# Kernel optimization log

Measured on AMD Instinct MI355X. Metric: run time of the kernel, lower is better.

## Reference

```python
import jax, jax.numpy as jnp
import numpy as np

NEG = -1e9  # max-semiring 'zero' / structural mask value


def _cky_max(pot, lengths):
    """Max-plus CKY inside pass (torch_struct CKY_CRF with MaxSemiring).

    pot: [B, N, N] label-maxed span potentials, pot[b, i, j] = score of span (i, j).
    Returns [B] best binary-tree score for each sequence of given length.
    betaA[b, i, w]      = best score of span starting at i with width w (span [i, i+w]).
    betaB[b, j, N-1-w]  = best score of span ending at j with width w.
    """
    B, N, _ = pot.shape
    term = jnp.diagonal(pot, axis1=1, axis2=2)  # [B, N] width-0 spans
    betaA = jnp.full((B, N, N), NEG, dtype=pot.dtype).at[:, :, 0].set(term)
    betaB = jnp.full((B, N, N), NEG, dtype=pot.dtype).at[:, :, N - 1].set(term)
    for w in range(1, N):
        Y = betaA[:, : N - w, :w]       # [B, N-w, w] left children, widths 0..w-1
        Z = betaB[:, w:, N - w:]        # [B, N-w, w] right children (matching splits)
        span = jnp.diagonal(pot, offset=w, axis1=1, axis2=2)  # [B, N-w] pot[b, i, i+w]
        new = jnp.max(Y + Z, axis=-1) + span
        betaA = betaA.at[:, : N - w, w].set(new)
        betaB = betaB.at[:, w:, N - w - 1].set(new)
    final = betaA[:, 0, :]  # [B, N]: final[b, l-1] = best tree over [0, l-1]
    return final[jnp.arange(B), lengths - 1]


def setup_inputs() -> dict:
    key = jax.random.key(0)
    k1, k2 = jax.random.split(key)
    B, N, L = 64, 128, 32
    logits = jax.random.normal(k1, (B, N, N, L), dtype=jnp.float32)
    labels = jax.random.randint(k2, (B, N, N), 0, L, dtype=jnp.int64)
    return {"logits": logits, "labels": labels}


def reference(logits, labels):
    B, N, _, L = logits.shape
    gold_event = jax.nn.one_hot(jnp.maximum(labels, 0), L, dtype=logits.dtype)
    logits = logits - logits[..., :1]
    lengths = jnp.sum(labels[:, 0, :] != -100, axis=-1)
    augment = 1.0 - gold_event
    # force_root_constituent=True: forbid non-constituent root span
    augment = augment.at[jnp.arange(B), 0, lengths - 1, 0].add(-1e9)
    pot = jnp.max(logits + augment, axis=-1)  # max-semiring sum over label dim
    pred_score = _cky_max(pot, lengths)                      # [B]
    gold_score = jnp.sum(logits * gold_event, axis=(1, 2, 3))  # [B]
    margin_losses = jax.nn.relu(pred_score - gold_score)
    return jnp.mean(margin_losses)
```

## Files before the change

### kernel.cpp

```cpp
#include <hip/hip_runtime.h>

#define BATCH 64
#define SEQ   128
#define NLAB  32
#define NEGF  -3.0e38f
#define PA    132

__device__ __forceinline__ void bar_k(int K) {
    switch (K) {
    case 0: asm volatile("s_waitcnt lgkmcnt(0)" ::: "memory"); break;
    case 1: asm volatile("s_waitcnt lgkmcnt(1)" ::: "memory"); break;
    case 2: asm volatile("s_waitcnt lgkmcnt(2)" ::: "memory"); break;
    case 3: asm volatile("s_waitcnt lgkmcnt(3)" ::: "memory"); break;
    case 4: asm volatile("s_waitcnt lgkmcnt(4)" ::: "memory"); break;
    case 5: asm volatile("s_waitcnt lgkmcnt(5)" ::: "memory"); break;
    case 6: asm volatile("s_waitcnt lgkmcnt(6)" ::: "memory"); break;
    default: asm volatile("s_waitcnt lgkmcnt(7)" ::: "memory"); break;
    }
    __builtin_amdgcn_s_barrier();
}

__global__ __launch_bounds__(256) void pot_gold_kernel(
    const float* __restrict__ logits, const int* __restrict__ labels,
    float* __restrict__ pot, float* __restrict__ gpart, float* __restrict__ out)
{
    const int tid = threadIdx.x;
    const int wave = tid >> 6, lane = tid & 63;
    __shared__ __align__(16) float LP[4 * 16 * 36];
    __shared__ float gred[4];
    __shared__ int s_len;
    float* W = LP + wave * (16 * 36);

    const int block_cell0 = blockIdx.x * 256;
    const int b = block_cell0 >> 14;
    const bool has_row0 = (blockIdx.x & 63) == 0;

    if (blockIdx.x == 0 && tid == 0) out[0] = 0.0f;

    if (has_row0 && tid < 64) {
        const size_t base = (size_t)b << 14;
        int cnt = (labels[base + tid] != -100) + (labels[base + 64 + tid] != -100);
        #pragma unroll
        for (int d = 32; d; d >>= 1) cnt += __shfl_down(cnt, d, 64);
        if (tid == 0) s_len = cnt;
    }
    __syncthreads();
    const int len = has_row0 ? s_len : -1;

    float gacc = 0.0f;
    const int wave_cell0 = block_cell0 + wave * 64;

    #pragma unroll
    for (int chunk = 0; chunk < 4; ++chunk) {
        const int c0 = wave_cell0 + chunk * 16;
        const float4* src = reinterpret_cast<const float4*>(logits) + ((size_t)c0 << 3);
        const float4 f0 = src[lane];
        const float4 f1 = src[lane + 64];
        const int lv = (lane < 16) ? labels[c0 + lane] : 0;

        {
            const int cA = lane >> 3, tA = lane & 7;
            *reinterpret_cast<float4*>(W + cA * 36 + tA * 4) = f0;
            const int q1 = lane + 64;
            const int cB = q1 >> 3, tB = q1 & 7;
            *reinterpret_cast<float4*>(W + cB * 36 + tB * 4) = f1;
        }
        const int c = lane >> 2, u = lane & 3;
        const float4 r0 = *reinterpret_cast<const float4*>(W + c * 36 + u * 8);
        const float4 r1 = *reinterpret_cast<const float4*>(W + c * 36 + u * 8 + 4);

        int lab = __shfl(lv, c, 64);
        if (lab < 0) lab = 0;
        const float l0 = __shfl(r0.x, c << 2, 64);

        const int cell = c0 + c;
        const int ci = (cell >> 7) & (SEQ - 1);
        const int cj = cell & (SEQ - 1);
        const bool special = (ci == 0) && (cj == len - 1);

        const float vv[8] = { r0.x, r0.y, r0.z, r0.w, r1.x, r1.y, r1.z, r1.w };
        float m = NEGF, g = 0.0f;
        #pragma unroll
        for (int e = 0; e < 8; ++e) {
            const int l = u * 8 + e;
            const float r = vv[e] - l0;
            const bool isg = (l == lab);
            g = isg ? r : g;
            float cand = r + (isg ? 0.0f : 1.0f);
            if (l == 0 && special) cand -= 1.0e9f;
            m = fmaxf(m, cand);
        }
        m = fmaxf(m, __shfl_xor(m, 1, 64));
        m = fmaxf(m, __shfl_xor(m, 2, 64));
        g += __shfl_xor(g, 1, 64);
        g += __shfl_xor(g, 2, 64);
        if (u == 0) {
            pot[cell] = m;
            gacc += g;
        }
    }

    #pragma unroll
    for (int d = 1; d < 64; d <<= 1) gacc += __shfl_xor(gacc, d, 64);
    if (lane == 0) gred[wave] = gacc;
    __syncthreads();
    if (tid == 0)
        gpart[blockIdx.x] = gred[0] + gred[1] + gred[2] + gred[3];
}

__global__ __launch_bounds__(512, 1) void cky_kernel(
    const float* __restrict__ pot, const float* __restrict__ gpart,
    const int* __restrict__ labels, float* __restrict__ out)
{
    const int b = blockIdx.x;
    const int tid = threadIdx.x;
    const float* p = pot + (size_t)b * SEQ * SEQ;

    __shared__ __align__(16) float A[SEQ * PA];
    __shared__ __align__(16) float Bt[SEQ * PA];
    __shared__ int s_len;
    __shared__ float s_gold;

    if (tid < 64) {
        const size_t base = (size_t)b << 14;
        int cnt = (labels[base + tid] != -100) + (labels[base + 64 + tid] != -100);
        #pragma unroll
        for (int d = 32; d; d >>= 1) cnt += __shfl_down(cnt, d, 64);
        if (tid == 0) s_len = cnt;
    } else if (tid < 128) {
        float g = gpart[b * 64 + (tid - 64)];
        #pragma unroll
        for (int d = 32; d; d >>= 1) g += __shfl_down(g, d, 64);
        if (tid == 64) s_gold = g;
    }

    {
        const float4* p4 = reinterpret_cast<const float4*>(p);
        float4 vb[8];
        #pragma unroll
        for (int t = 0; t < 8; ++t) vb[t] = p4[tid + 512 * t];
        #pragma unroll
        for (int t = 0; t < 8; ++t) {
            const int qi = tid + 512 * t;
            const int i0 = qi >> 5;
            const int j0 = (qi & 31) << 2;
            const float vv[4] = { vb[t].x, vb[t].y, vb[t].z, vb[t].w };
            #pragma unroll
            for (int c2 = 0; c2 < 4; ++c2) {
                const int j = j0 + c2;
                if (j >= i0) {
                    A[i0 * PA + (j - i0)] = vv[c2];
                    Bt[j * PA + (SEQ - 1 - (j - i0))] = vv[c2];
                }
            }
        }
    }
    __syncthreads();

    const int i = tid >> 2, s = tid & 3;
    float alo[16], av[16], pv[16], md[16];
    float bo_p[16], bf_p[12];

    #pragma unroll
    for (int t = 0; t < 4; ++t) {
        const float4 v = *reinterpret_cast<const float4*>(&A[i * PA + 4 * t]);
        pv[4*t] = v.x; pv[4*t+1] = v.y; pv[4*t+2] = v.z; pv[4*t+3] = v.w;
    }
    av[0] = pv[0];
    #pragma unroll
    for (int d = 1; d < 16; ++d) {
        const int j = i + d;
        const int tf = (d - 1) >> 2;
        const int jr = (j < SEQ) ? j : SEQ - 1;
        float bff[4];
        {
            const float4 u = *reinterpret_cast<const float4*>(&Bt[jr * PA + 124 - 4 * tf]);
            bff[0] = u.w; bff[1] = u.z; bff[2] = u.y; bff[3] = u.x;
        }
        float e[16];
        #pragma unroll
        for (int m = 0; m < d; ++m)
            e[m] = av[d - 1 - m] + ((m < 4 * tf) ? bo_p[m] : bff[m - 4 * tf]);
        #pragma unroll
        for (int stp = 1; stp < 16; stp <<= 1) {
            #pragma unroll
            for (int m = 0; m + stp < d; m += 2 * stp)
                e[m] = fmaxf(e[m], e[m + stp]);
        }
        const float val = e[0] + pv[d];
        av[d] = val;
        if (j < SEQ && s == 0) {
            A[i * PA + d] = val;
            Bt[j * PA + (SEQ - 1 - d)] = val;
        }
        __builtin_amdgcn_sched_barrier(0);
        if (d < 15) {
            int jp = j + 1; if (jp >= SEQ) jp = SEQ - 1;
            const int tfn = d >> 2;
            #pragma unroll
            for (int t = 0; t < 4; ++t) {
                if (t < tfn) {
                    const float4 v = *reinterpret_cast<const float4*>(&Bt[jp * PA + 124 - 4 * t]);
                    bo_p[4*t] = v.w; bo_p[4*t+1] = v.z; bo_p[4*t+2] = v.y; bo_p[4*t+3] = v.x;
                }
            }
            bar_k(tfn);
        } else {
            bar_k(0);
        }
    }
    #pragma unroll
    for (int k = 0; k < 16; ++k) alo[k] = av[k];

    for (int W = 16; W < SEQ; W += 16) {
        #pragma unroll
        for (int t = 0; t < 4; ++t) {
            const float4 v = *reinterpret_cast<const float4*>(&A[i * PA + W + 4 * t]);
            pv[4*t] = v.x; pv[4*t+1] = v.y; pv[4*t+2] = v.z; pv[4*t+3] = v.w;
        }
        #pragma unroll
        for (int d = 0; d < 16; ++d) md[d] = NEGF;

        {
            const int k0 = s << 2;
            const float4 a = *reinterpret_cast<const float4*>(&A[i * PA + k0]);
            const float aa[4] = { a.x, a.y, a.z, a.w };
            #pragma unroll
            for (int d = 0; d < 16; ++d) {
                const int j = i + W + d;
                if (j < SEQ) {
                    const float* bp = &Bt[j * PA + (SEQ - W - d) + k0];
                    float b0, b1, b2, b3;
                    if ((d & 3) == 0) {
                        const float4 v = *reinterpret_cast<const float4*>(bp);
                        b0 = v.x; b1 = v.y; b2 = v.z; b3 = v.w;
                    } else if ((d & 3) == 2) {
                        const float2 v0 = *reinterpret_cast<const float2*>(bp);
                        const float2 v1 = *reinterpret_cast<const float2*>(bp + 2);
                        b0 = v0.x; b1 = v0.y; b2 = v1.x; b3 = v1.y;
                    } else {
                        b0 = bp[0];
                        const float2 v = *reinterpret_cast<const float2*>(bp + 1);
                        b1 = v.x; b2 = v.y; b3 = bp[3];
                    }
                    const float a0 = (k0 + 0 >= d) ? aa[0] : NEGF;
                    const float a1 = (k0 + 1 >= d) ? aa[1] : NEGF;
                    const float a2 = (k0 + 2 >= d) ? aa[2] : NEGF;
                    const float a3 = (k0 + 3 >= d) ? aa[3] : NEGF;
                    md[d] = fmaxf(md[d], fmaxf(fmaxf(a0 + b0, a1 + b1),
                                               fmaxf(a2 + b2, a3 + b3)));
                }
            }
        }
        for (int q = s + 4; q < (W >> 2); q += 4) {
            const int k0 = q << 2;
            const float4 a = *reinterpret_cast<const float4*>(&A[i * PA + k0]);
            #pragma unroll
            for (int d = 0; d < 16; ++d) {
                const int j = i + W + d;
                if (j < SEQ) {
                    const float* bp = &Bt[j * PA + (SEQ - W - d) + k0];
                    float b0, b1, b2, b3;
                    if ((d & 3) == 0) {
                        const float4 v = *reinterpret_cast<const float4*>(bp);
                        b0 = v.x; b1 = v.y; b2 = v.z; b3 = v.w;
                    } else if ((d & 3) == 2) {
                        const float2 v0 = *reinterpret_cast<const float2*>(bp);
                        const float2 v1 = *reinterpret_cast<const float2*>(bp + 2);
                        b0 = v0.x; b1 = v0.y; b2 = v1.x; b3 = v1.y;
                    } else {
                        b0 = bp[0];
                        const float2 v = *reinterpret_cast<const float2*>(bp + 1);
                        b1 = v.x; b2 = v.y; b3 = bp[3];
                    }
                    md[d] = fmaxf(md[d], fmaxf(fmaxf(a.x + b0, a.y + b1),
                                               fmaxf(a.z + b2, a.w + b3)));
                }
            }
        }
        #pragma unroll
        for (int d = 0; d < 16; ++d) {
            md[d] = fmaxf(md[d], __shfl_xor(md[d], 1, 4));
            md[d] = fmaxf(md[d], __shfl_xor(md[d], 2, 4));
        }

        {
            const int j = i + W;
            const float val = md[0] + pv[0];
            av[0] = val;
            if (j < SEQ && s == 0) {
                A[i * PA + W] = val;
                Bt[j * PA + (SEQ - 1 - W)] = val;
            }
            __builtin_amdgcn_sched_barrier(0);
            int jp = j + 1; if (jp >= SEQ) jp = SEQ - 1;
            const float4 v = *reinterpret_cast<const float4*>(&Bt[jp * PA + 124]);
            bo_p[0] = v.w; bo_p[1] = v.z; bo_p[2] = v.y; bo_p[3] = v.x;
            bar_k(1);
        }
        #pragma unroll
        for (int d = 1; d < 16; ++d) {
            const int w = W + d;
            const int j = i + w;
            const int tf = (d - 1) >> 2;
            const int jr = (j < SEQ) ? j : SEQ - 1;
            float bff[4];
            {
                const float4 u = *reinterpret_cast<const float4*>(&Bt[jr * PA + 124 - W - 4 * tf]);
                bff[0] = u.w; bff[1] = u.z; bff[2] = u.y; bff[3] = u.x;
            }
            float e[30];
            #pragma unroll
            for (int m = 0; m < d; ++m)
                e[m] = av[d - 1 - m] + bo_p[m];
            #pragma unroll
            for (int m = 0; m < d; ++m)
                e[d + m] = alo[d - 1 - m] + ((m < 4 * tf) ? bf_p[m] : bff[m - 4 * tf]);
            #pragma unroll
            for (int stp = 1; stp < 32; stp <<= 1) {
                #pragma unroll
                for (int m = 0; m + stp < 2 * d; m += 2 * stp)
                    e[m] = fmaxf(e[m], e[m + stp]);
            }
            const float val = fmaxf(md[d], e[0]) + pv[d];
            av[d] = val;
            if (j < SEQ && s == 0) {
                A[i * PA + w] = val;
                Bt[j * PA + (SEQ - 1 - w)] = val;
            }
            __builtin_amdgcn_sched_barrier(0);
            if (d < 15) {
                int jp = j + 1; if (jp >= SEQ) jp = SEQ - 1;
                const int NQn = (d + 4) >> 2;
                #pragma unroll
                for (int t = 0; t < 4; ++t) {
                    if (t < NQn) {
                        const float4 v = *reinterpret_cast<const float4*>(&Bt[jp * PA + 124 - 4 * t]);
                        bo_p[4*t] = v.w; bo_p[4*t+1] = v.z; bo_p[4*t+2] = v.y; bo_p[4*t+3] = v.x;
                    }
                }
                const int tfn = d >> 2;
                #pragma unroll
                for (int t = 0; t < 3; ++t) {
                    if (t < tfn) {
                        const float4 v = *reinterpret_cast<const float4*>(&Bt[jp * PA + 124 - W - 4 * t]);
                        bf_p[4*t] = v.w; bf_p[4*t+1] = v.z; bf_p[4*t+2] = v.y; bf_p[4*t+3] = v.x;
                    }
                }
                bar_k(NQn + tfn);
            } else {
                bar_k(0);
            }
        }
    }

    if (tid == 0) {
        const int len = s_len;
        const float pred = A[len - 1];
        const float margin = fmaxf(pred - s_gold, 0.0f);
        atomicAdd(out, margin * (1.0f / (float)BATCH));
    }
}

extern "C" void kernel_launch(void* const* d_in, const int* in_sizes, int n_in,
                              void* d_out, int out_size, void* d_ws, size_t ws_size,
                              hipStream_t stream) {
    const float* logits = (const float*)d_in[0];
    const int* labels = (const int*)d_in[1];
    float* out = (float*)d_out;

    float* pot = (float*)d_ws;
    float* gpart = pot + (size_t)BATCH * SEQ * SEQ;

    pot_gold_kernel<<<BATCH * SEQ * SEQ / 256, 256, 0, stream>>>(
        logits, labels, pot, gpart, out);
    cky_kernel<<<BATCH, 512, 0, stream>>>(pot, gpart, labels, out);
}
```

Baseline: 258.0 us.

## Split CKY diagonal split-point reduction across the 4 lanes per span with DPP max

In the serial diagonal recurrence of the CKY kernel, each of the 4 lanes assigned to a span now handles one quarter of the split points (4 each) instead of every lane redundantly computing all of them. Partial maxima are combined with DPP quad permutes instead of ds_swizzle-based shuffles, and the two LDS result writes are spread over two lanes. This cuts per-step ALU work and the per-lane LDS prefetch count on the latency-bound critical path. In exchange, each step now pays a cross-lane reduction and carries more per-lane branching on s.

New measurement: 256.5 us. No clear change (-0.6%).

```diff
diff --git a/kernel.cpp b/kernel.cpp
--- a/kernel.cpp
+++ b/kernel.cpp
@@ -18,6 +18,15 @@
     default: asm volatile("s_waitcnt lgkmcnt(7)" ::: "memory"); break;
     }
     __builtin_amdgcn_s_barrier();
+}
+
+__device__ __forceinline__ float qmax1(float v) {
+    int t = __builtin_amdgcn_update_dpp(0, __float_as_int(v), 0xB1, 0xF, 0xF, true);
+    return fmaxf(v, __int_as_float(t));
+}
+__device__ __forceinline__ float qmax2(float v) {
+    int t = __builtin_amdgcn_update_dpp(0, __float_as_int(v), 0x4E, 0xF, 0xF, true);
+    return fmaxf(v, __int_as_float(t));
 }
 
 __global__ __launch_bounds__(256) void pot_gold_kernel(
@@ -159,7 +168,36 @@
 
     const int i = tid >> 2, s = tid & 3;
     float alo[16], av[16], pv[16], md[16];
-    float bo_p[16], bf_p[12];
+    float boq[4], bfq[4];
+
+#define C0_BODY(Sv)                                                           \
+    if (s == (Sv)) {                                                          \
+        _Pragma("unroll")                                                     \
+        for (int e = 0; e < 4; ++e) {                                         \
+            const int m = 4 * (Sv) + e;                                       \
+            if (m < d) {                                                      \
+                const float bv = ((Sv) == ((d - 1) >> 2))                     \
+                    ? ((e == 0) ? fq.w : (e == 1) ? fq.z : (e == 2) ? fq.y : fq.x) \
+                    : boq[e];                                                 \
+                part = fmaxf(part, av[d - 1 - m] + bv);                       \
+            }                                                                 \
+        }                                                                     \
+    }
+
+#define CH_BODY(Sv)                                                           \
+    if (s == (Sv)) {                                                          \
+        _Pragma("unroll")                                                     \
+        for (int e = 0; e < 4; ++e) {                                         \
+            const int m = 4 * (Sv) + e;                                       \
+            if (m < d) {                                                      \
+                part = fmaxf(part, av[d - 1 - m] + boq[e]);                   \
+                const float bv = ((Sv) == ((d - 1) >> 2))                     \
+                    ? ((e == 0) ? fq.w : (e == 1) ? fq.z : (e == 2) ? fq.y : fq.x) \
+                    : bfq[e];                                                 \
+                part = fmaxf(part, alo[d - 1 - m] + bv);                      \
+            }                                                                 \
+        }                                                                     \
+    }
 
     #pragma unroll
     for (int t = 0; t < 4; ++t) {
@@ -167,44 +205,36 @@
         pv[4*t] = v.x; pv[4*t+1] = v.y; pv[4*t+2] = v.z; pv[4*t+3] = v.w;
     }
     av[0] = pv[0];
+
+    {
+        const int jp = (i + 1 < SEQ) ? (i + 1) : (SEQ - 1);
+        const float4 bv = *reinterpret_cast<const float4*>(&Bt[jp * PA + 124 - 4 * s]);
+        boq[0] = bv.w; boq[1] = bv.z; boq[2] = bv.y; boq[3] = bv.x;
+    }
+
     #pragma unroll
     for (int d = 1; d < 16; ++d) {
         const int j = i + d;
-        const int tf = (d - 1) >> 2;
         const int jr = (j < SEQ) ? j : SEQ - 1;
-        float bff[4];
-        {
-            const float4 u = *reinterpret_cast<const float4*>(&Bt[jr * PA + 124 - 4 * tf]);
-            bff[0] = u.w; bff[1] = u.z; bff[2] = u.y; bff[3] = u.x;
-        }
-        float e[16];
-        #pragma unroll
-        for (int m = 0; m < d; ++m)
-            e[m] = av[d - 1 - m] + ((m < 4 * tf) ? bo_p[m] : bff[m - 4 * tf]);
-        #pragma unroll
-        for (int stp = 1; stp < 16; stp <<= 1) {
-            #pragma unroll
-            for (int m = 0; m + stp < d; m += 2 * stp)
-                e[m] = fmaxf(e[m], e[m + stp]);
-        }
-        const float val = e[0] + pv[d];
+        const float4 fq = *reinterpret_cast<const float4*>(&Bt[jr * PA + 124 - 4 * ((d - 1) >> 2)]);
+        float part = NEGF;
+        C0_BODY(0)
+        C0_BODY(1)
+        C0_BODY(2)
+        C0_BODY(3)
+        part = qmax2(qmax1(part));
+        const float val = part + pv[d];
         av[d] = val;
-        if (j < SEQ && s == 0) {
-            A[i * PA + d] = val;
-            Bt[j * PA + (SEQ - 1 - d)] = val;
+        if (j < SEQ && s < 2) {
+            float* pw = (s == 0) ? &A[i * PA + d] : &Bt[j * PA + (SEQ - 1 - d)];
+            *pw = val;
         }
         __builtin_amdgcn_sched_barrier(0);
         if (d < 15) {
-            int jp = j + 1; if (jp >= SEQ) jp = SEQ - 1;
-            const int tfn = d >> 2;
-            #pragma unroll
-            for (int t = 0; t < 4; ++t) {
-                if (t < tfn) {
-                    const float4 v = *reinterpret_cast<const float4*>(&Bt[jp * PA + 124 - 4 * t]);
-                    bo_p[4*t] = v.w; bo_p[4*t+1] = v.z; bo_p[4*t+2] = v.y; bo_p[4*t+3] = v.x;
-                }
-            }
-            bar_k(tfn);
+            const int jp = (j + 1 < SEQ) ? (j + 1) : (SEQ - 1);
+            const float4 bv = *reinterpret_cast<const float4*>(&Bt[jp * PA + 124 - 4 * s]);
+            boq[0] = bv.w; boq[1] = bv.z; boq[2] = bv.y; boq[3] = bv.x;
+            bar_k(1);
         } else {
             bar_k(0);
         }
@@ -280,74 +310,52 @@
         }
         #pragma unroll
         for (int d = 0; d < 16; ++d) {
-            md[d] = fmaxf(md[d], __shfl_xor(md[d], 1, 4));
-            md[d] = fmaxf(md[d], __shfl_xor(md[d], 2, 4));
+            md[d] = qmax2(qmax1(md[d]));
         }
 
         {
             const int j = i + W;
             const float val = md[0] + pv[0];
             av[0] = val;
-            if (j < SEQ && s == 0) {
-                A[i * PA + W] = val;
-                Bt[j * PA + (SEQ - 1 - W)] = val;
+            if (j < SEQ && s < 2) {
+                float* pw = (s == 0) ? &A[i * PA + W] : &Bt[j * PA + (SEQ - 1 - W)];
+                *pw = val;
             }
             __builtin_amdgcn_sched_barrier(0);
-            int jp = j + 1; if (jp >= SEQ) jp = SEQ - 1;
-            const float4 v = *reinterpret_cast<const float4*>(&Bt[jp * PA + 124]);
-            bo_p[0] = v.w; bo_p[1] = v.z; bo_p[2] = v.y; bo_p[3] = v.x;
-            bar_k(1);
+            const int jp = (j + 1 < SEQ) ? (j + 1) : (SEQ - 1);
+            const float4 bv = *reinterpret_cast<const float4*>(&Bt[jp * PA + 124 - 4 * s]);
+            const float4 fv = *reinterpret_cast<const float4*>(&Bt[jp * PA + 124 - W - 4 * s]);
+            boq[0] = bv.w; boq[1] = bv.z; boq[2] = bv.y; boq[3] = bv.x;
+            bfq[0] = fv.w; bfq[1] = fv.z; bfq[2] = fv.y; bfq[3] = fv.x;
+            bar_k(2);
         }
         #pragma unroll
         for (int d = 1; d < 16; ++d) {
             const int w = W + d;
             const int j = i + w;
-            const int tf = (d - 1) >> 2;
             const int jr = (j < SEQ) ? j : SEQ - 1;
-            float bff[4];
-            {
-                const float4 u = *reinterpret_cast<const float4*>(&Bt[jr * PA + 124 - W - 4 * tf]);
-                bff[0] = u.w; bff[1] = u.z; bff[2] = u.y; bff[3] = u.x;
-            }
-            float e[30];
-            #pragma unroll
-            for (int m = 0; m < d; ++m)
-                e[m] = av[d - 1 - m] + bo_p[m];
-            #pragma unroll
-            for (int m = 0; m < d; ++m)
-                e[d + m] = alo[d - 1 - m] + ((m < 4 * tf) ? bf_p[m] : bff[m - 4 * tf]);
-            #pragma unroll
-            for (int stp = 1; stp < 32; stp <<= 1) {
-                #pragma unroll
-                for (int m = 0; m + stp < 2 * d; m += 2 * stp)
-                    e[m] = fmaxf(e[m], e[m + stp]);
-            }
-            const float val = fmaxf(md[d], e[0]) + pv[d];
+            const float4 fq = *reinterpret_cast<const float4*>(
+                &Bt[jr * PA + 124 - W - 4 * ((d - 1) >> 2)]);
+            float part = NEGF;
+            CH_BODY(0)
+            CH_BODY(1)
+            CH_BODY(2)
+            CH_BODY(3)
+            part = qmax2(qmax1(part));
+            const float val = fmaxf(part, md[d]) + pv[d];
             av[d] = val;
-            if (j < SEQ && s == 0) {
-                A[i * PA + w] = val;
-                Bt[j * PA + (SEQ - 1 - w)] = val;
+            if (j < SEQ && s < 2) {
+                float* pw = (s == 0) ? &A[i * PA + w] : &Bt[j * PA + (SEQ - 1 - w)];
+                *pw = val;
             }
             __builtin_amdgcn_sched_barrier(0);
             if (d < 15) {
-                int jp = j + 1; if (jp >= SEQ) jp = SEQ - 1;
-                const int NQn = (d + 4) >> 2;
-                #pragma unroll
-                for (int t = 0; t < 4; ++t) {
-                    if (t < NQn) {
-                        const float4 v = *reinterpret_cast<const float4*>(&Bt[jp * PA + 124 - 4 * t]);
-                        bo_p[4*t] = v.w; bo_p[4*t+1] = v.z; bo_p[4*t+2] = v.y; bo_p[4*t+3] = v.x;
-                    }
-                }
-                const int tfn = d >> 2;
-                #pragma unroll
-                for (int t = 0; t < 3; ++t) {
-                    if (t < tfn) {
-                        const float4 v = *reinterpret_cast<const float4*>(&Bt[jp * PA + 124 - W - 4 * t]);
-                        bf_p[4*t] = v.w; bf_p[4*t+1] = v.z; bf_p[4*t+2] = v.y; bf_p[4*t+3] = v.x;
-                    }
-                }
-                bar_k(NQn + tfn);
+                const int jp = (j + 1 < SEQ) ? (j + 1) : (SEQ - 1);
+                const float4 bv = *reinterpret_cast<const float4*>(&Bt[jp * PA + 124 - 4 * s]);
+                const float4 fv = *reinterpret_cast<const float4*>(&Bt[jp * PA + 124 - W - 4 * s]);
+                boq[0] = bv.w; boq[1] = bv.z; boq[2] = bv.y; boq[3] = bv.x;
+                bfq[0] = fv.w; bfq[1] = fv.z; bfq[2] = fv.y; bfq[3] = fv.x;
+                bar_k(2);
             } else {
                 bar_k(0);
             }
@@ -360,6 +368,8 @@
         const float margin = fmaxf(pred - s_gold, 0.0f);
         atomicAdd(out, margin * (1.0f / (float)BATCH));
     }
+#undef C0_BODY
+#undef CH_BODY
 }
 
 extern "C" void kernel_launch(void* const* d_in, const int* in_sizes, int n_in,
```
